# Kernel tuning notes

Measured on AMD Instinct MI355X. Metric: run time of the kernel, lower is better.

Reference implementation:

```python
import jax, jax.numpy as jnp
import numpy as np
from jax import lax

N = 100000      # nodes
E = 1600000     # edges
T = 8           # timesteps
DS, DT = 10, 20 # static / temporal features
GH = 64         # gnn_hidden
LH = 64         # lstm_hidden
EC = 64         # end_channels
OC = 1          # out_channels
EPS = 1e-5


def setup_inputs() -> dict:
    key = jax.random.key(0)
    ks = jax.random.split(key, 20)
    g = lambda i, shape, s=0.05: jax.random.normal(ks[i], shape, jnp.float32) * s
    return {
        "x": jax.random.normal(ks[0], (N, DS + DT, T), jnp.float32),
        "edge_index": jax.random.randint(ks[1], (2, E), 0, N, jnp.int64),
        # static encoder (computed in forward but unused downstream, kept for faithfulness)
        "W_static": g(2, (GH, DS)), "b_static": g(3, (GH,)),
        # LSTMCell: input_size = DT + GH, hidden = LH; gate order i,f,g,o
        "W_ih": g(4, (4 * LH, DT + GH)), "W_hh": g(5, (4 * LH, LH)),
        "b_ih": g(6, (4 * LH,)), "b_hh": g(7, (4 * LH,)),
        # GraphConv(lstm_hidden -> gnn_hidden): lin_rel (with bias) on aggregated msgs + lin_root (no bias)
        "W_rel": g(8, (GH, LH)), "b_rel": g(9, (GH,)), "W_root": g(10, (GH, LH)),
        # BatchNorm1d(GH+LH)
        "gamma": jnp.ones((GH + LH,), jnp.float32), "beta": jnp.zeros((GH + LH,), jnp.float32),
        # head: linear1(128->EC), linear2(EC->128), output_layer(128->OC)
        "W1": g(11, (EC, GH + LH)), "b1": g(12, (EC,)),
        "W2": g(13, (GH + LH, EC)), "b2": g(14, (GH + LH,)),
        "W_out": g(15, (OC, GH + LH)), "b_out": g(16, (OC,)),
    }


def reference(x, edge_index, W_static, b_static, W_ih, W_hh, b_ih, b_hh,
              W_rel, b_rel, W_root, gamma, beta, W1, b1, W2, b2, W_out, b_out):
    src, dst = edge_index[0], edge_index[1]
    x_static = x[:, :DS, 0]                      # [N, DS]
    x_temporal = x[:, DS:DS + DT, :]             # [N, DT, T]
    static_embed = x_static @ W_static.T + b_static  # computed but unused (matches source)

    xt_seq = jnp.transpose(x_temporal, (2, 0, 1))  # [T, N, DT]
    h0 = jnp.zeros((N, GH), jnp.float32)
    c0 = jnp.zeros((N, GH), jnp.float32)

    def step(carry, x_t):
        h, c = carry
        # GraphConv: sum-aggregate neighbor h, then linear (linear commutes with sum)
        agg = jax.ops.segment_sum(h[src], dst, num_segments=N)   # [N, LH]
        gnn_out = agg @ W_rel.T + b_rel + h @ W_root.T           # [N, GH]
        inp = jnp.concatenate([x_t, gnn_out], axis=1)            # [N, DT+GH]
        gates = inp @ W_ih.T + b_ih + h @ W_hh.T + b_hh          # [N, 4*LH]
        i, f, g_, o = jnp.split(gates, 4, axis=1)
        c_new = jax.nn.sigmoid(f) * c + jax.nn.sigmoid(i) * jnp.tanh(g_)
        h_new = jax.nn.sigmoid(o) * jnp.tanh(c_new)
        return (h_new, c_new), gnn_out

    (h, c), gnn_outs = lax.scan(step, (h0, c0), xt_seq)
    gnn_out = gnn_outs[-1]  # gnn output computed at the last timestep (pre-update h)

    fused = jnp.concatenate([h, gnn_out], axis=1)                # [N, GH+LH]
    # BatchNorm1d, training-mode batch statistics (dropout p set to 0)
    mean = fused.mean(axis=0)
    var = fused.var(axis=0)
    normed = (fused - mean) * lax.rsqrt(var + EPS) * gamma + beta
    h1 = jax.nn.relu(normed @ W1.T + b1)
    hidden = jax.nn.relu(h1 @ W2.T + b2)
    out = jax.nn.sigmoid(hidden @ W_out.T + b_out)               # binary task -> sigmoid
    return out
```

## Files before the change

kernel.cpp:

```cpp
#include <hip/hip_runtime.h>

#define NN 100000
#define NE 1600000
#define TT 8
#define KF 160
#define XSTR 24
#define HISTB 6250
#define NRANGE 8
#define RSPAN 12500

typedef __attribute__((ext_vector_type(8))) short bf16x8;
typedef __attribute__((ext_vector_type(4))) float f32x4;
typedef unsigned int uint_;
typedef unsigned short ushort_;
typedef __attribute__((ext_vector_type(4))) uint_ u32x4;

__device__ __forceinline__ float sigf(float x) { return 1.f / (1.f + __expf(-x)); }
__device__ __forceinline__ float tanhf_(float x) { return 1.f - 2.f / (__expf(2.f * x) + 1.f); }
__device__ __forceinline__ ushort_ f2b(float f) {
    uint_ u = __float_as_uint(f);
    u += 0x7fff + ((u >> 16) & 1);
    return (ushort_)(u >> 16);
}
__device__ __forceinline__ float bl(uint_ u) { return __uint_as_float(u << 16); }
__device__ __forceinline__ float bh(uint_ u) { return __uint_as_float(u & 0xffff0000u); }
__device__ __forceinline__ void acc8(float* a, uint4 v) {
    a[0] += bl(v.x); a[1] += bh(v.x); a[2] += bl(v.y); a[3] += bh(v.y);
    a[4] += bl(v.z); a[5] += bh(v.z); a[6] += bl(v.w); a[7] += bh(v.w);
}
__device__ __forceinline__ uint_ pk(float a, float b) {
    return (uint_)f2b(a) | ((uint_)f2b(b) << 16);
}
__device__ __forceinline__ uint4 ntld16(const void* p) {
    u32x4 v = __builtin_nontemporal_load((const u32x4*)p);
    return make_uint4(v[0], v[1], v[2], v[3]);
}

__global__ void k_detect(const int* __restrict__ ei, int* flag) {
    int i = blockIdx.x * 256 + threadIdx.x;
    if (ei[2 * i + 1] != 0) atomicOr(flag, 1);
}

__global__ void k_hist_xt(const int* __restrict__ ei, const int* __restrict__ flag, int* cnt,
                          const float* __restrict__ x, ushort_* __restrict__ xT) {
    int b = blockIdx.x;
    if (b < HISTB) {
        int e = b * 256 + threadIdx.x;
        if (e >= NE) return;
        int is32 = *flag;
        int d = is32 ? ei[NE + e] : ei[2 * (NE + e)];
        atomicAdd(&cnt[d], 1);
    } else {
        if (!xT) return;
        int i = (b - HISTB) * 256 + threadIdx.x;
        if (i >= NN * XSTR) return;
        int n = i / XSTR, kk = i - n * XSTR;
        if (kk < 20) {
            const float* xp = x + (size_t)n * 240 + (10 + kk) * 8;
#pragma unroll
            for (int t = 0; t < 8; t++) xT[(size_t)t * NN * XSTR + i] = f2b(xp[t]);
        } else {
#pragma unroll
            for (int t = 0; t < 8; t++) xT[(size_t)t * NN * XSTR + i] = 0;
        }
    }
}

__global__ void k_scanblk(const int* __restrict__ cnt, int* off, int* bsum) {
    __shared__ int tmp[1024];
    int i = blockIdx.x * 1024 + threadIdx.x;
    int v = (i < NN) ? cnt[i] : 0;
    tmp[threadIdx.x] = v;
    __syncthreads();
    for (int d = 1; d < 1024; d <<= 1) {
        int t = (threadIdx.x >= d) ? tmp[threadIdx.x - d] : 0;
        __syncthreads();
        tmp[threadIdx.x] += t;
        __syncthreads();
    }
    if (i < NN) off[i + 1] = tmp[threadIdx.x];
    if (threadIdx.x == 1023) bsum[blockIdx.x] = tmp[1023];
}

__global__ void k_scantop(int* bsum, int nb) {
    if (threadIdx.x == 0) {
        int run = 0;
        for (int b = 0; b < nb; b++) { int t = bsum[b]; bsum[b] = run; run += t; }
    }
}

__global__ void k_scanadd(int* off, const int* __restrict__ bsum) {
    int i = blockIdx.x * 1024 + threadIdx.x;
    if (i < NN) off[i + 1] += bsum[blockIdx.x];
    if (i == 0) off[0] = 0;
}

__global__ void k_scatter(const int* __restrict__ ei, const int* __restrict__ flag,
                          int* cursor, int* csr) {
    int b = blockIdx.x;
    int range = b & (NRANGE - 1), chunk = b >> 3;
    int e = chunk * 256 + threadIdx.x;
    if (e >= NE) return;
    int is32 = *flag;
    int d = is32 ? ei[NE + e] : ei[2 * (NE + e)];
    if (d / RSPAN != range) return;
    int s = is32 ? ei[e] : ei[2 * e];
    int pos = atomicAdd(&cursor[d], 1);
    csr[pos] = s;
}

__global__ void k_prep(const float* __restrict__ W_ih, const float* __restrict__ W_hh,
                       const float* __restrict__ b_ih, const float* __restrict__ b_hh,
                       const float* __restrict__ W_rel, const float* __restrict__ b_rel,
                       const float* __restrict__ W_root, ushort_* WgB, float* bgp) {
    int n = threadIdx.x;
    int k = blockIdx.x;
    if (k < KF) {
        float v = 0.f;
        if (n < 256) {
            int w = n >> 6, g = (n >> 4) & 3, j = w * 16 + (n & 15);
            int row = g * 64 + j;
            if (k < 20) {
                v = W_ih[row * 84 + k];
            } else if (k >= 24 && k < 88) {
                int kk = k - 24;
                float a = 0.f;
                for (int m = 0; m < 64; m++) a += W_ih[row * 84 + 20 + m] * W_rel[m * 64 + kk];
                v = a;
            } else if (k >= 88 && k < 152) {
                int kk = k - 88;
                float a = W_hh[row * 64 + kk];
                for (int m = 0; m < 64; m++) a += W_ih[row * 84 + 20 + m] * W_root[m * 64 + kk];
                v = a;
            }
        } else {
            int j = n - 256;
            if (k >= 24 && k < 88) v = W_rel[j * 64 + (k - 24)];
            else if (k >= 88 && k < 152) v = W_root[j * 64 + (k - 88)];
        }
        WgB[(size_t)n * KF + k] = f2b(v);
    } else {
        if (n < 256) {
            int j = n >> 2, g = n & 3;
            int row = g * 64 + j;
            float a = b_ih[row] + b_hh[row];
            for (int m = 0; m < 64; m++) a += W_ih[row * 84 + 20 + m] * b_rel[m];
            bgp[n] = a;
        } else {
            bgp[n] = b_rel[n - 256];
        }
    }
}

template <bool LAST>
__device__ __forceinline__ void step_body(const float* __restrict__ x,
                                          const ushort_* __restrict__ xT,
                                          const int* __restrict__ off,
                                          const int* __restrict__ csr,
                                          const ushort_* __restrict__ hbR,
                                          ushort_* __restrict__ hbW,
                                          float* __restrict__ hf,
                                          float* __restrict__ c,
                                          const ushort_* __restrict__ WgB,
                                          const float* __restrict__ bgp,
                                          float* __restrict__ gnn,
                                          float* __restrict__ sums,
                                          float* __restrict__ sumsq, int t) {
    __shared__ __align__(16) ushort_ Zs[64 * 168];
    __shared__ __align__(16) float Cs0[64 * 64];
    __shared__ int sPerm[64];
    __shared__ int sE0[64], sE1[64];
    const int tid = threadIdx.x;
    const int nblk = blockIdx.x * 64;
    const int w = tid >> 6, lane = tid & 63;
    const int q = lane >> 4, l16 = lane & 15;

    if (tid < 64) {
        int n_g = nblk + tid;
        int e0 = (n_g < NN) ? off[n_g] : 0;
        int e1 = (n_g < NN) ? off[n_g + 1] : 0;
        sE0[tid] = e0; sE1[tid] = e1;
        int key = ((e1 - e0) << 6) | tid;
        int rank = 0;
#pragma unroll
        for (int m = 0; m < 64; m++) rank += (__shfl(key, m, 64) > key) ? 1 : 0;
        sPerm[rank] = tid;
    }

#pragma unroll
    for (int i = 0; i < 3; ++i) {
        int slot = tid + 256 * i;
        int n = slot / 12, oo = slot - n * 12;
        int n_g = nblk + n;
        uint4 z = make_uint4(0, 0, 0, 0);
        if (n_g < NN) {
            if (oo < 3) {
                if (xT) {
                    z = ntld16(xT + ((size_t)t * NN + n_g) * XSTR + oo * 8);
                } else {
                    const float* xp = x + (size_t)n_g * 240 + 80 + (size_t)oo * 64 + t;
                    uint_ r[4];
#pragma unroll
                    for (int p = 0; p < 4; p++) {
                        int k0 = oo * 8 + p * 2;
                        ushort_ b0 = (k0 < 20) ? f2b(xp[p * 16]) : (ushort_)0;
                        ushort_ b1 = (k0 + 1 < 20) ? f2b(xp[p * 16 + 8]) : (ushort_)0;
                        r[p] = (uint_)b0 | ((uint_)b1 << 16);
                    }
                    z = make_uint4(r[0], r[1], r[2], r[3]);
                }
            } else if (oo < 11) {
                if (t > 0)
                    z = *(const uint4*)(hbR + (size_t)n_g * 64 + (oo - 3) * 8);
            }
        }
        int oct = (oo < 3) ? oo : ((oo < 11) ? (oo + 8) : 19);
        *(uint4*)(Zs + n * 168 + oct * 8) = z;
    }
    __syncthreads();

    {
        int slot = tid >> 3;
        int l8 = tid & 7;
#pragma unroll
        for (int pass = 0; pass < 2; ++pass) {
            int nn = sPerm[pass ? (63 - slot) : slot];
            float a[8];
#pragma unroll
            for (int i = 0; i < 8; i++) a[i] = 0.f;
            if (t > 0) {
                int e0 = sE0[nn], e1 = sE1[nn];
                int e = e0;
                if (e + 8 <= e1) {
                    uint4 v[8];
#pragma unroll
                    for (int i = 0; i < 8; i++)
                        v[i] = *(const uint4*)(hbR + (size_t)csr[e + i] * 64 + l8 * 8);
                    e += 8;
                    for (; e + 8 <= e1; e += 8) {
#pragma unroll
                        for (int i = 0; i < 4; i++) {
                            acc8(a, v[i]);
                            v[i] = *(const uint4*)(hbR + (size_t)csr[e + i] * 64 + l8 * 8);
                        }
#pragma unroll
                        for (int i = 4; i < 8; i++) {
                            acc8(a, v[i]);
                            v[i] = *(const uint4*)(hbR + (size_t)csr[e + i] * 64 + l8 * 8);
                        }
                    }
#pragma unroll
                    for (int i = 0; i < 8; i++) acc8(a, v[i]);
                }
                for (; e < e1; e++) {
                    uint4 v0 = *(const uint4*)(hbR + (size_t)csr[e] * 64 + l8 * 8);
                    acc8(a, v0);
                }
            }
            uint4 o;
            o.x = pk(a[0], a[1]); o.y = pk(a[2], a[3]);
            o.z = pk(a[4], a[5]); o.w = pk(a[6], a[7]);
            *(uint4*)(Zs + nn * 168 + 24 + l8 * 8) = o;
        }
    }

    if (t > 0) {
        const float* cb = c + (size_t)nblk * 64;
        const int lim = (NN - nblk) * 64;
#pragma unroll
        for (int k2 = 0; k2 < 4; ++k2) {
            int f = (tid + 256 * k2) * 4;
            float4 v = make_float4(0.f, 0.f, 0.f, 0.f);
            if (f < lim) v = *(const float4*)(cb + f);
            *(float4*)(Cs0 + f) = v;
        }
    }
    __syncthreads();

    const int j = w * 16 + l16;
    float sh = 0.f, sh2 = 0.f, sg = 0.f, sg2 = 0.f;

    if (LAST) {
        f32x4 accg[4];
#pragma unroll
        for (int mt = 0; mt < 4; mt++) accg[mt] = (f32x4)(0.f);
#pragma unroll
        for (int kt = 0; kt < 5; ++kt) {
            bf16x8 bfg = *(const bf16x8*)(WgB + (size_t)(256 + w * 16 + l16) * KF + kt * 32 + q * 8);
#pragma unroll
            for (int mt = 0; mt < 4; mt++) {
                bf16x8 af = *(const bf16x8*)(Zs + (mt * 16 + l16) * 168 + kt * 32 + q * 8);
                accg[mt] = __builtin_amdgcn_mfma_f32_16x16x32_bf16(af, bfg, accg[mt], 0, 0, 0);
            }
        }
        const float brl = bgp[256 + j];
#pragma unroll
        for (int mt = 0; mt < 4; ++mt)
#pragma unroll
            for (int r = 0; r < 4; ++r) {
                int node = nblk + mt * 16 + q * 4 + r;
                if (node < NN) {
                    float gn = accg[mt][r] + brl;
                    gnn[(size_t)node * 64 + j] = gn;
                    sg += gn; sg2 += gn * gn;
                }
            }
    }

    f32x4 acc[4][4];
#pragma unroll
    for (int mt = 0; mt < 4; mt++)
#pragma unroll
        for (int nt = 0; nt < 4; nt++) acc[mt][nt] = (f32x4)(0.f);

#pragma unroll
    for (int kt = 0; kt < 5; ++kt) {
        bf16x8 af[4], bf[4];
#pragma unroll
        for (int mt = 0; mt < 4; mt++)
            af[mt] = *(const bf16x8*)(Zs + (mt * 16 + l16) * 168 + kt * 32 + q * 8);
#pragma unroll
        for (int nt = 0; nt < 4; nt++) {
            int n = w * 64 + nt * 16 + l16;
            bf[nt] = *(const bf16x8*)(WgB + (size_t)n * KF + kt * 32 + q * 8);
        }
#pragma unroll
        for (int mt = 0; mt < 4; mt++)
#pragma unroll
            for (int nt = 0; nt < 4; nt++)
                acc[mt][nt] = __builtin_amdgcn_mfma_f32_16x16x32_bf16(af[mt], bf[nt], acc[mt][nt], 0, 0, 0);
    }

    const f32x4 bias = *(const f32x4*)(bgp + j * 4);

    __syncthreads();
    ushort_* Hs   = Zs;
    float*   CsLo = (float*)(Zs + 4096);

    float cnHi[8];
#pragma unroll
    for (int mt = 0; mt < 4; ++mt) {
#pragma unroll
        for (int r = 0; r < 4; ++r) {
            int nloc = mt * 16 + q * 4 + r;
            int node = nblk + nloc;
            float cn = 0.f, hn = 0.f;
            if (node < NN) {
                size_t idx = (size_t)node * 64 + j;
                float iv = sigf(acc[mt][0][r] + bias.x);
                float fv = sigf(acc[mt][1][r] + bias.y);
                float gv = tanhf_(acc[mt][2][r] + bias.z);
                float ov = sigf(acc[mt][3][r] + bias.w);
                float cold = (t > 0) ? Cs0[nloc * 64 + j] : 0.f;
                cn = fv * cold + iv * gv;
                hn = ov * tanhf_(cn);
                if (LAST) {
                    hf[idx] = hn;
                    sh += hn; sh2 += hn * hn;
                }
            }
            Hs[nloc * 64 + j] = f2b(hn);
            if (mt < 2) CsLo[nloc * 64 + j] = cn;
            else        cnHi[(mt - 2) * 4 + r] = cn;
        }
    }
    __syncthreads();
#pragma unroll
    for (int i = 0; i < 2; ++i) {
        int s = tid + 256 * i;
        {
            int n = s >> 3, part = s & 7;
            if (nblk + n < NN)
                *(uint4*)(hbW + (size_t)(nblk + n) * 64 + part * 8) =
                    *(const uint4*)(Hs + n * 64 + part * 8);
        }
        {
            int n = s >> 4, part = s & 15;
            if (nblk + n < NN)
                *(float4*)(c + (size_t)(nblk + n) * 64 + part * 4) =
                    *(const float4*)(CsLo + n * 64 + part * 4);
        }
    }
    __syncthreads();
    float* CsHi = (float*)Zs;
#pragma unroll
    for (int mt = 2; mt < 4; ++mt)
#pragma unroll
        for (int r = 0; r < 4; ++r) {
            int nloc = mt * 16 + q * 4 + r;
            CsHi[(nloc - 32) * 64 + j] = cnHi[(mt - 2) * 4 + r];
        }
    __syncthreads();
#pragma unroll
    for (int i = 0; i < 2; ++i) {
        int s = tid + 256 * i;
        int n = 32 + (s >> 4), part = s & 15;
        if (nblk + n < NN)
            *(float4*)(c + (size_t)(nblk + n) * 64 + part * 4) =
                *(const float4*)(CsHi + (n - 32) * 64 + part * 4);
    }

    if (LAST) {
#pragma unroll
        for (int d = 16; d < 64; d <<= 1) {
            sh += __shfl_xor(sh, d, 64);
            sh2 += __shfl_xor(sh2, d, 64);
            sg += __shfl_xor(sg, d, 64);
            sg2 += __shfl_xor(sg2, d, 64);
        }
        if (q == 0) {
            atomicAdd(&sums[j], sh);
            atomicAdd(&sumsq[j], sh2);
            atomicAdd(&sums[64 + j], sg);
            atomicAdd(&sumsq[64 + j], sg2);
        }
    }
}

__global__ __launch_bounds__(256, 4) void k_step(const float* __restrict__ x,
                                                 const ushort_* __restrict__ xT,
                                                 const int* __restrict__ off,
                                                 const int* __restrict__ csr,
                                                 const ushort_* __restrict__ hbR,
                                                 ushort_* __restrict__ hbW,
                                                 float* __restrict__ hf,
                                                 float* __restrict__ c,
                                                 const ushort_* __restrict__ WgB,
                                                 const float* __restrict__ bgp, int t) {
    step_body<false>(x, xT, off, csr, hbR, hbW, hf, c, WgB, bgp, nullptr, nullptr, nullptr, t);
}

__global__ __launch_bounds__(256, 4) void k_stepL(const float* __restrict__ x,
                                                  const ushort_* __restrict__ xT,
                                                  const int* __restrict__ off,
                                                  const int* __restrict__ csr,
                                                  const ushort_* __restrict__ hbR,
                                                  ushort_* __restrict__ hbW,
                                                  float* __restrict__ hf,
                                                  float* __restrict__ c,
                                                  const ushort_* __restrict__ WgB,
                                                  const float* __restrict__ bgp,
                                                  float* __restrict__ gnn,
                                                  float* __restrict__ sums,
                                                  float* __restrict__ sumsq, int t) {
    step_body<true>(x, xT, off, csr, hbR, hbW, hf, c, WgB, bgp, gnn, sums, sumsq, t);
}

__global__ __launch_bounds__(256) void k_head(const float* __restrict__ hf,
                                              const float* __restrict__ gnn,
                                              const float* __restrict__ sums,
                                              const float* __restrict__ sumsq,
                                              const float* __restrict__ gamma,
                                              const float* __restrict__ beta,
                                              const float* __restrict__ W1,
                                              const float* __restrict__ b1,
                                              const float* __restrict__ W2,
                                              const float* __restrict__ b2,
                                              const float* __restrict__ W_out,
                                              const float* __restrict__ b_out,
                                              float* __restrict__ out) {
    __shared__ __align__(16) ushort_ Zs[64 * 168];
    __shared__ __align__(16) ushort_ W1s[64 * 168];
    __shared__ __align__(16) ushort_ W2s[128 * 72];
    __shared__ __align__(16) ushort_ H1s[64 * 72];
    __shared__ float ab[256];
    __shared__ float Obuf[4][64];
    const int tid = threadIdx.x;
    const int w = tid >> 6, lane = tid & 63;
    const int q = lane >> 4, l16 = lane & 15;

    if (tid < 128) {
        float mean = sums[tid] / (float)NN;
        float var = sumsq[tid] / (float)NN - mean * mean;
        float a = gamma[tid] * rsqrtf(var + 1e-5f);
        ab[tid] = a;
        ab[128 + tid] = beta[tid] - mean * a;
    }
#pragma unroll
    for (int i = 0; i < 8; ++i) {
        int slot = tid + 256 * i;
        int jj = slot >> 5, k4 = slot & 31;
        float4 v = *(const float4*)(W1 + (size_t)jj * 128 + k4 * 4);
        *(uint2*)(W1s + jj * 168 + k4 * 4) = make_uint2(pk(v.x, v.y), pk(v.z, v.w));
    }
#pragma unroll
    for (int i = 0; i < 8; ++i) {
        int slot = tid + 256 * i;
        int jj = slot >> 4, k4 = slot & 15;
        float4 v = *(const float4*)(W2 + (size_t)jj * 64 + k4 * 4);
        *(uint2*)(W2s + jj * 72 + k4 * 4) = make_uint2(pk(v.x, v.y), pk(v.z, v.w));
    }
    const int j1 = w * 16 + l16;
    const float bb1 = b1[j1];
    const int j2a = (w * 2) * 16 + l16, j2b = (w * 2 + 1) * 16 + l16;
    const float bb2a = b2[j2a], bb2b = b2[j2b];
    const float woa = W_out[j2a], wob = W_out[j2b];
    const float bo = b_out[0];
    __syncthreads();

    const int NTILE = (NN + 63) / 64;
    for (int tile = blockIdx.x; tile < NTILE; tile += gridDim.x) {
        const int nblk = tile * 64;
#pragma unroll
        for (int i = 0; i < 8; ++i) {
            int slot = tid + 256 * i;
            int n = slot >> 5, f4 = slot & 31;
            int n_g = nblk + n;
            uint2 z = make_uint2(0, 0);
            if (n_g < NN) {
                const float* src = (f4 < 16) ? (hf + (size_t)n_g * 64 + f4 * 4)
                                             : (gnn + (size_t)n_g * 64 + (f4 - 16) * 4);
                float4 v = *(const float4*)src;
                int F = f4 * 4;
                z = make_uint2(pk(v.x * ab[F] + ab[128 + F], v.y * ab[F + 1] + ab[129 + F]),
                               pk(v.z * ab[F + 2] + ab[130 + F], v.w * ab[F + 3] + ab[131 + F]));
            }
            *(uint2*)(Zs + n * 168 + f4 * 4) = z;
        }
        __syncthreads();
        f32x4 acc1[4];
#pragma unroll
        for (int mt = 0; mt < 4; mt++) acc1[mt] = (f32x4)(0.f);
#pragma unroll
        for (int kt = 0; kt < 4; ++kt) {
            bf16x8 bfw = *(const bf16x8*)(W1s + j1 * 168 + kt * 32 + q * 8);
#pragma unroll
            for (int mt = 0; mt < 4; mt++) {
                bf16x8 af = *(const bf16x8*)(Zs + (mt * 16 + l16) * 168 + kt * 32 + q * 8);
                acc1[mt] = __builtin_amdgcn_mfma_f32_16x16x32_bf16(af, bfw, acc1[mt], 0, 0, 0);
            }
        }
#pragma unroll
        for (int mt = 0; mt < 4; mt++)
#pragma unroll
            for (int r = 0; r < 4; r++) {
                int nloc = mt * 16 + q * 4 + r;
                H1s[nloc * 72 + j1] = f2b(fmaxf(acc1[mt][r] + bb1, 0.f));
            }
        __syncthreads();
        f32x4 acc2[4][2];
#pragma unroll
        for (int mt = 0; mt < 4; mt++)
#pragma unroll
            for (int nt = 0; nt < 2; nt++) acc2[mt][nt] = (f32x4)(0.f);
#pragma unroll
        for (int kt = 0; kt < 2; ++kt) {
            bf16x8 bfa = *(const bf16x8*)(W2s + j2a * 72 + kt * 32 + q * 8);
            bf16x8 bfb = *(const bf16x8*)(W2s + j2b * 72 + kt * 32 + q * 8);
#pragma unroll
            for (int mt = 0; mt < 4; mt++) {
                bf16x8 af = *(const bf16x8*)(H1s + (mt * 16 + l16) * 72 + kt * 32 + q * 8);
                acc2[mt][0] = __builtin_amdgcn_mfma_f32_16x16x32_bf16(af, bfa, acc2[mt][0], 0, 0, 0);
                acc2[mt][1] = __builtin_amdgcn_mfma_f32_16x16x32_bf16(af, bfb, acc2[mt][1], 0, 0, 0);
            }
        }
#pragma unroll
        for (int mt = 0; mt < 4; mt++) {
#pragma unroll
            for (int r = 0; r < 4; r++) {
                float p = fmaxf(acc2[mt][0][r] + bb2a, 0.f) * woa +
                          fmaxf(acc2[mt][1][r] + bb2b, 0.f) * wob;
#pragma unroll
                for (int d = 1; d < 16; d <<= 1) p += __shfl_xor(p, d, 64);
                if (l16 == 0) Obuf[w][mt * 16 + q * 4 + r] = p;
            }
        }
        __syncthreads();
        if (tid < 64) {
            int n_g = nblk + tid;
            if (n_g < NN) {
                float s = Obuf[0][tid] + Obuf[1][tid] + Obuf[2][tid] + Obuf[3][tid];
                out[n_g] = sigf(s + bo);
            }
        }
        __syncthreads();
    }
}

extern "C" void kernel_launch(void* const* d_in, const int* in_sizes, int n_in,
                              void* d_out, int out_size, void* d_ws, size_t ws_size,
                              hipStream_t stream) {
    const float* x      = (const float*)d_in[0];
    const int*   ei     = (const int*)d_in[1];
    const float* W_ih   = (const float*)d_in[4];
    const float* W_hh   = (const float*)d_in[5];
    const float* b_ih   = (const float*)d_in[6];
    const float* b_hh   = (const float*)d_in[7];
    const float* W_rel  = (const float*)d_in[8];
    const float* b_rel  = (const float*)d_in[9];
    const float* W_root = (const float*)d_in[10];
    const float* gamma  = (const float*)d_in[11];
    const float* beta   = (const float*)d_in[12];
    const float* W1     = (const float*)d_in[13];
    const float* b1     = (const float*)d_in[14];
    const float* W2     = (const float*)d_in[15];
    const float* b2     = (const float*)d_in[16];
    const float* W_out  = (const float*)d_in[17];
    const float* b_out  = (const float*)d_in[18];
    float* out = (float*)d_out;

    char* ws = (char*)d_ws;
    size_t o = 0;
    auto carve = [&](size_t bytes) { char* p = ws + o; o += (bytes + 255) & ~(size_t)255; return p; };
    int*     off   = (int*)carve((NN + 1) * 4);
    int*     cnt   = (int*)carve(NN * 4);
    int*     bsum  = (int*)carve(128 * 4);
    int*     flag  = (int*)carve(256);
    int*     csr   = (int*)carve((size_t)NE * 4);
    float*   hf    = (float*)carve((size_t)NN * 64 * 4);
    float*   c     = (float*)carve((size_t)NN * 64 * 4);
    float*   gnn   = (float*)carve((size_t)NN * 64 * 4);
    ushort_* hbA   = (ushort_*)carve((size_t)NN * 64 * 2);
    ushort_* hbB   = (ushort_*)carve((size_t)NN * 64 * 2);
    ushort_* WgB   = (ushort_*)carve((size_t)320 * KF * 2);
    float*   bgp   = (float*)carve(320 * 4);
    float*   sums  = (float*)carve(128 * 4);
    float*   sumsq = (float*)carve(128 * 4);
    ushort_* xT = nullptr;
    size_t need_xt = (size_t)TT * NN * XSTR * 2;
    if (o + need_xt + 256 <= ws_size) xT = (ushort_*)carve(need_xt);

    const int nscan = (NN + 1023) / 1024;
    const int xtb = xT ? (NN * XSTR + 255) / 256 : 0;

    hipMemsetAsync(flag, 0, 4, stream);
    hipMemsetAsync(cnt, 0, NN * 4, stream);
    k_detect<<<16, 256, 0, stream>>>(ei, flag);
    k_hist_xt<<<HISTB + xtb, 256, 0, stream>>>(ei, flag, cnt, x, xT);
    k_scanblk<<<nscan, 1024, 0, stream>>>(cnt, off, bsum);
    k_scantop<<<1, 64, 0, stream>>>(bsum, nscan);
    k_scanadd<<<nscan, 1024, 0, stream>>>(off, bsum);
    hipMemcpyAsync(cnt, off, NN * 4, hipMemcpyDeviceToDevice, stream);
    k_scatter<<<(NE / 256) * NRANGE, 256, 0, stream>>>(ei, flag, cnt, csr);

    hipMemsetAsync(sums, 0, 1024, stream);
    k_prep<<<KF + 1, 320, 0, stream>>>(W_ih, W_hh, b_ih, b_hh, W_rel, b_rel, W_root, WgB, bgp);

    const int ngates = (NN + 63) / 64;
    for (int t = 0; t < TT; ++t) {
        ushort_* hbR = (t & 1) ? hbB : hbA;
        ushort_* hbW = (t & 1) ? hbA : hbB;
        if (t == TT - 1)
            k_stepL<<<ngates, 256, 0, stream>>>(x, xT, off, csr, hbR, hbW, hf, c,
                                                WgB, bgp, gnn, sums, sumsq, t);
        else
            k_step<<<ngates, 256, 0, stream>>>(x, xT, off, csr, hbR, hbW, hf, c,
                                               WgB, bgp, t);
    }

    k_head<<<512, 256, 0, stream>>>(hf, gnn, sums, sumsq, gamma, beta,
                                    W1, b1, W2, b2, W_out, b_out, out);
}
```

Baseline: 897.1 us.

## Split neighbor gather into separate kernel and tile xT transpose through shared memory

Each timestep's fused step kernel is split into a dedicated gather kernel, which sums neighbor hidden states into a bf16 aggregate buffer at higher occupancy, and a gates kernel that reads that buffer. This separates the latency-bound irregular gather from the MFMA gate computation, which ran at lower occupancy. The price is an extra NN×64 bf16 buffer written and read per step, plus more launches. The xT preprocessing now loads x rows with coalesced float4 reads into shared memory and writes 16-byte packed outputs instead of doing scalar strided accesses.

```diff
diff --git a/kernel.cpp b/kernel.cpp
--- a/kernel.cpp
+++ b/kernel.cpp
@@ -43,25 +43,46 @@
 
 __global__ void k_hist_xt(const int* __restrict__ ei, const int* __restrict__ flag, int* cnt,
                           const float* __restrict__ x, ushort_* __restrict__ xT) {
+    __shared__ float xs[32][164];
     int b = blockIdx.x;
+    int tid = threadIdx.x;
     if (b < HISTB) {
-        int e = b * 256 + threadIdx.x;
+        int e = b * 256 + tid;
         if (e >= NE) return;
         int is32 = *flag;
         int d = is32 ? ei[NE + e] : ei[2 * (NE + e)];
         atomicAdd(&cnt[d], 1);
     } else {
         if (!xT) return;
-        int i = (b - HISTB) * 256 + threadIdx.x;
-        if (i >= NN * XSTR) return;
-        int n = i / XSTR, kk = i - n * XSTR;
-        if (kk < 20) {
-            const float* xp = x + (size_t)n * 240 + (10 + kk) * 8;
-#pragma unroll
-            for (int t = 0; t < 8; t++) xT[(size_t)t * NN * XSTR + i] = f2b(xp[t]);
-        } else {
-#pragma unroll
-            for (int t = 0; t < 8; t++) xT[(size_t)t * NN * XSTR + i] = 0;
+        int nblk = (b - HISTB) * 32;
+#pragma unroll
+        for (int i = 0; i < 5; ++i) {
+            int slot = tid + 256 * i;
+            int n = slot / 40, f4 = slot - n * 40;
+            int n_g = nblk + n;
+            float4 v = make_float4(0.f, 0.f, 0.f, 0.f);
+            if (n_g < NN) v = *(const float4*)(x + (size_t)n_g * 240 + 80 + f4 * 4);
+            *(float4*)(&xs[n][f4 * 4]) = v;
+        }
+        __syncthreads();
+#pragma unroll
+        for (int i = 0; i < 3; ++i) {
+            int slot = tid + 256 * i;
+            int tt = slot / 96, p = slot - tt * 96;
+            int n = p / 3, kk0 = (p - n * 3) * 8;
+            int n_g = nblk + n;
+            if (n_g < NN) {
+                uint_ r[4];
+#pragma unroll
+                for (int u = 0; u < 4; u++) {
+                    int k0 = kk0 + u * 2;
+                    float f0 = (k0 < 20) ? xs[n][k0 * 8 + tt] : 0.f;
+                    float f1 = (k0 + 1 < 20) ? xs[n][(k0 + 1) * 8 + tt] : 0.f;
+                    r[u] = pk(f0, f1);
+                }
+                *(uint4*)(xT + (size_t)tt * NN * XSTR + (size_t)n_g * XSTR + kk0) =
+                    make_uint4(r[0], r[1], r[2], r[3]);
+            }
         }
     }
 }
@@ -152,45 +173,73 @@
     }
 }
 
+__global__ __launch_bounds__(256, 8) void k_gather(const int* __restrict__ off,
+                                                   const int* __restrict__ csr,
+                                                   const ushort_* __restrict__ hbR,
+                                                   ushort_* __restrict__ aggB) {
+    int node = blockIdx.x * 32 + (threadIdx.x >> 3);
+    int l8 = threadIdx.x & 7;
+    if (node >= NN) return;
+    int e0 = off[node], e1 = off[node + 1];
+    float a[8];
+#pragma unroll
+    for (int i = 0; i < 8; i++) a[i] = 0.f;
+    int e = e0;
+    if (e + 8 <= e1) {
+        uint4 v[8];
+#pragma unroll
+        for (int i = 0; i < 8; i++)
+            v[i] = *(const uint4*)(hbR + (size_t)csr[e + i] * 64 + l8 * 8);
+        e += 8;
+        for (; e + 8 <= e1; e += 8) {
+#pragma unroll
+            for (int i = 0; i < 4; i++) {
+                acc8(a, v[i]);
+                v[i] = *(const uint4*)(hbR + (size_t)csr[e + i] * 64 + l8 * 8);
+            }
+#pragma unroll
+            for (int i = 4; i < 8; i++) {
+                acc8(a, v[i]);
+                v[i] = *(const uint4*)(hbR + (size_t)csr[e + i] * 64 + l8 * 8);
+            }
+        }
+#pragma unroll
+        for (int i = 0; i < 8; i++) acc8(a, v[i]);
+    }
+    for (; e < e1; e++) {
+        uint4 v0 = *(const uint4*)(hbR + (size_t)csr[e] * 64 + l8 * 8);
+        acc8(a, v0);
+    }
+    uint4 o;
+    o.x = pk(a[0], a[1]); o.y = pk(a[2], a[3]);
+    o.z = pk(a[4], a[5]); o.w = pk(a[6], a[7]);
+    *(uint4*)(aggB + (size_t)node * 64 + l8 * 8) = o;
+}
+
 template <bool LAST>
-__device__ __forceinline__ void step_body(const float* __restrict__ x,
-                                          const ushort_* __restrict__ xT,
-                                          const int* __restrict__ off,
-                                          const int* __restrict__ csr,
-                                          const ushort_* __restrict__ hbR,
-                                          ushort_* __restrict__ hbW,
-                                          float* __restrict__ hf,
-                                          float* __restrict__ c,
-                                          const ushort_* __restrict__ WgB,
-                                          const float* __restrict__ bgp,
-                                          float* __restrict__ gnn,
-                                          float* __restrict__ sums,
-                                          float* __restrict__ sumsq, int t) {
+__device__ __forceinline__ void gates_body(const ushort_* __restrict__ xT,
+                                           const float* __restrict__ x,
+                                           const ushort_* __restrict__ aggB,
+                                           const ushort_* __restrict__ hbR,
+                                           ushort_* __restrict__ hbW,
+                                           float* __restrict__ hf,
+                                           float* __restrict__ c,
+                                           const ushort_* __restrict__ WgB,
+                                           const float* __restrict__ bgp,
+                                           float* __restrict__ gnn,
+                                           float* __restrict__ sums,
+                                           float* __restrict__ sumsq, int t) {
     __shared__ __align__(16) ushort_ Zs[64 * 168];
     __shared__ __align__(16) float Cs0[64 * 64];
-    __shared__ int sPerm[64];
-    __shared__ int sE0[64], sE1[64];
     const int tid = threadIdx.x;
     const int nblk = blockIdx.x * 64;
     const int w = tid >> 6, lane = tid & 63;
     const int q = lane >> 4, l16 = lane & 15;
 
-    if (tid < 64) {
-        int n_g = nblk + tid;
-        int e0 = (n_g < NN) ? off[n_g] : 0;
-        int e1 = (n_g < NN) ? off[n_g + 1] : 0;
-        sE0[tid] = e0; sE1[tid] = e1;
-        int key = ((e1 - e0) << 6) | tid;
-        int rank = 0;
-#pragma unroll
-        for (int m = 0; m < 64; m++) rank += (__shfl(key, m, 64) > key) ? 1 : 0;
-        sPerm[rank] = tid;
-    }
-
-#pragma unroll
-    for (int i = 0; i < 3; ++i) {
+#pragma unroll
+    for (int i = 0; i < 5; ++i) {
         int slot = tid + 256 * i;
-        int n = slot / 12, oo = slot - n * 12;
+        int n = slot / 20, oo = slot - n * 20;
         int n_g = nblk + n;
         uint4 z = make_uint4(0, 0, 0, 0);
         if (n_g < NN) {
@@ -210,58 +259,12 @@
                     z = make_uint4(r[0], r[1], r[2], r[3]);
                 }
             } else if (oo < 11) {
-                if (t > 0)
-                    z = *(const uint4*)(hbR + (size_t)n_g * 64 + (oo - 3) * 8);
-            }
-        }
-        int oct = (oo < 3) ? oo : ((oo < 11) ? (oo + 8) : 19);
-        *(uint4*)(Zs + n * 168 + oct * 8) = z;
-    }
-    __syncthreads();
-
-    {
-        int slot = tid >> 3;
-        int l8 = tid & 7;
-#pragma unroll
-        for (int pass = 0; pass < 2; ++pass) {
-            int nn = sPerm[pass ? (63 - slot) : slot];
-            float a[8];
-#pragma unroll
-            for (int i = 0; i < 8; i++) a[i] = 0.f;
-            if (t > 0) {
-                int e0 = sE0[nn], e1 = sE1[nn];
-                int e = e0;
-                if (e + 8 <= e1) {
-                    uint4 v[8];
-#pragma unroll
-                    for (int i = 0; i < 8; i++)
-                        v[i] = *(const uint4*)(hbR + (size_t)csr[e + i] * 64 + l8 * 8);
-                    e += 8;
-                    for (; e + 8 <= e1; e += 8) {
-#pragma unroll
-                        for (int i = 0; i < 4; i++) {
-                            acc8(a, v[i]);
-                            v[i] = *(const uint4*)(hbR + (size_t)csr[e + i] * 64 + l8 * 8);
-                        }
-#pragma unroll
-                        for (int i = 4; i < 8; i++) {
-                            acc8(a, v[i]);
-                            v[i] = *(const uint4*)(hbR + (size_t)csr[e + i] * 64 + l8 * 8);
-                        }
-                    }
-#pragma unroll
-                    for (int i = 0; i < 8; i++) acc8(a, v[i]);
-                }
-                for (; e < e1; e++) {
-                    uint4 v0 = *(const uint4*)(hbR + (size_t)csr[e] * 64 + l8 * 8);
-                    acc8(a, v0);
-                }
-            }
-            uint4 o;
-            o.x = pk(a[0], a[1]); o.y = pk(a[2], a[3]);
-            o.z = pk(a[4], a[5]); o.w = pk(a[6], a[7]);
-            *(uint4*)(Zs + nn * 168 + 24 + l8 * 8) = o;
-        }
+                if (t > 0) z = *(const uint4*)(aggB + (size_t)n_g * 64 + (oo - 3) * 8);
+            } else if (oo < 19) {
+                if (t > 0) z = *(const uint4*)(hbR + (size_t)n_g * 64 + (oo - 11) * 8);
+            }
+        }
+        *(uint4*)(Zs + n * 168 + oo * 8) = z;
     }
 
     if (t > 0) {
@@ -417,33 +420,31 @@
     }
 }
 
-__global__ __launch_bounds__(256, 4) void k_step(const float* __restrict__ x,
-                                                 const ushort_* __restrict__ xT,
-                                                 const int* __restrict__ off,
-                                                 const int* __restrict__ csr,
-                                                 const ushort_* __restrict__ hbR,
-                                                 ushort_* __restrict__ hbW,
-                                                 float* __restrict__ hf,
-                                                 float* __restrict__ c,
-                                                 const ushort_* __restrict__ WgB,
-                                                 const float* __restrict__ bgp, int t) {
-    step_body<false>(x, xT, off, csr, hbR, hbW, hf, c, WgB, bgp, nullptr, nullptr, nullptr, t);
-}
-
-__global__ __launch_bounds__(256, 4) void k_stepL(const float* __restrict__ x,
-                                                  const ushort_* __restrict__ xT,
-                                                  const int* __restrict__ off,
-                                                  const int* __restrict__ csr,
+__global__ __launch_bounds__(256, 4) void k_gates(const ushort_* __restrict__ xT,
+                                                  const float* __restrict__ x,
+                                                  const ushort_* __restrict__ aggB,
                                                   const ushort_* __restrict__ hbR,
                                                   ushort_* __restrict__ hbW,
                                                   float* __restrict__ hf,
                                                   float* __restrict__ c,
                                                   const ushort_* __restrict__ WgB,
-                                                  const float* __restrict__ bgp,
-                                                  float* __restrict__ gnn,
-                                                  float* __restrict__ sums,
-                                                  float* __restrict__ sumsq, int t) {
-    step_body<true>(x, xT, off, csr, hbR, hbW, hf, c, WgB, bgp, gnn, sums, sumsq, t);
+                                                  const float* __restrict__ bgp, int t) {
+    gates_body<false>(xT, x, aggB, hbR, hbW, hf, c, WgB, bgp, nullptr, nullptr, nullptr, t);
+}
+
+__global__ __launch_bounds__(256, 4) void k_gatesL(const ushort_* __restrict__ xT,
+                                                   const float* __restrict__ x,
+                                                   const ushort_* __restrict__ aggB,
+                                                   const ushort_* __restrict__ hbR,
+                                                   ushort_* __restrict__ hbW,
+                                                   float* __restrict__ hf,
+                                                   float* __restrict__ c,
+                                                   const ushort_* __restrict__ WgB,
+                                                   const float* __restrict__ bgp,
+                                                   float* __restrict__ gnn,
+                                                   float* __restrict__ sums,
+                                                   float* __restrict__ sumsq, int t) {
+    gates_body<true>(xT, x, aggB, hbR, hbW, hf, c, WgB, bgp, gnn, sums, sumsq, t);
 }
 
 __global__ __launch_bounds__(256) void k_head(const float* __restrict__ hf,
@@ -612,6 +613,7 @@
     float*   gnn   = (float*)carve((size_t)NN * 64 * 4);
     ushort_* hbA   = (ushort_*)carve((size_t)NN * 64 * 2);
     ushort_* hbB   = (ushort_*)carve((size_t)NN * 64 * 2);
+    ushort_* aggB  = (ushort_*)carve((size_t)NN * 64 * 2);
     ushort_* WgB   = (ushort_*)carve((size_t)320 * KF * 2);
     float*   bgp   = (float*)carve(320 * 4);
     float*   sums  = (float*)carve(128 * 4);
@@ -621,7 +623,7 @@
     if (o + need_xt + 256 <= ws_size) xT = (ushort_*)carve(need_xt);
 
     const int nscan = (NN + 1023) / 1024;
-    const int xtb = xT ? (NN * XSTR + 255) / 256 : 0;
+    const int xtb = xT ? (NN + 31) / 32 : 0;
 
     hipMemsetAsync(flag, 0, 4, stream);
     hipMemsetAsync(cnt, 0, NN * 4, stream);
@@ -637,15 +639,18 @@
     k_prep<<<KF + 1, 320, 0, stream>>>(W_ih, W_hh, b_ih, b_hh, W_rel, b_rel, W_root, WgB, bgp);
 
     const int ngates = (NN + 63) / 64;
+    const int ngath = (NN + 31) / 32;
     for (int t = 0; t < TT; ++t) {
         ushort_* hbR = (t & 1) ? hbB : hbA;
         ushort_* hbW = (t & 1) ? hbA : hbB;
+        if (t > 0)
+            k_gather<<<ngath, 256, 0, stream>>>(off, csr, hbR, aggB);
         if (t == TT - 1)
-            k_stepL<<<ngates, 256, 0, stream>>>(x, xT, off, csr, hbR, hbW, hf, c,
-                                                WgB, bgp, gnn, sums, sumsq, t);
+            k_gatesL<<<ngates, 256, 0, stream>>>(xT, x, aggB, hbR, hbW, hf, c,
+                                                 WgB, bgp, gnn, sums, sumsq, t);
         else
-            k_step<<<ngates, 256, 0, stream>>>(x, xT, off, csr, hbR, hbW, hf, c,
-                                               WgB, bgp, t);
+            k_gates<<<ngates, 256, 0, stream>>>(xT, x, aggB, hbR, hbW, hf, c,
+                                                WgB, bgp, t);
     }
 
     k_head<<<512, 256, 0, stream>>>(hf, gnn, sums, sumsq, gamma, beta,
```

Result: slower. 1.121 ms (+24.9%).
